# Kernel tuning notes

Measured on AMD Instinct MI355X. Metric: run time of the kernel, lower is better.

Reference implementation:

```python
import jax, jax.numpy as jnp
import numpy as np
import math

IN_C, OUT_C, K, STYLE_DIM = 512, 512, 3, 512
BATCH, H, W = 16, 64, 64
EPS = 1e-8
CONV_SCALE = 1.0 / math.sqrt(IN_C * K * K)   # fan_in scale
MOD_SCALE = 1.0 / math.sqrt(STYLE_DIM)       # EqualLinear scale (lr_mul=1)


def setup_inputs() -> dict:
    key = jax.random.key(0)
    k1, k2, k3, k4 = jax.random.split(key, 4)
    return {
        "input": jax.random.normal(k1, (BATCH, IN_C, H, W), dtype=jnp.float32),
        "style": jax.random.normal(k2, (BATCH, STYLE_DIM), dtype=jnp.float32),
        "weight": jax.random.normal(k3, (1, OUT_C, IN_C, K, K), dtype=jnp.float32),
        "mod_weight": jax.random.normal(k4, (IN_C, STYLE_DIM), dtype=jnp.float32),
        "mod_bias": jnp.ones((IN_C,), dtype=jnp.float32),  # bias_init=1
    }


def reference(input, style, weight, mod_weight, mod_bias):
    b = input.shape[0]
    # EqualLinear modulation: style -> per-sample per-in-channel scale
    s = style @ (mod_weight * MOD_SCALE).T + mod_bias          # [B, IN_C]
    # Modulate base weight per sample
    w = CONV_SCALE * weight * s[:, None, :, None, None]        # [B, OUT_C, IN_C, K, K]
    # Demodulation
    demod = jax.lax.rsqrt(jnp.sum(w * w, axis=(2, 3, 4)) + EPS)  # [B, OUT_C]
    w = w * demod[:, :, None, None, None]
    # Grouped conv with groups=batch == per-sample conv; vmap over batch
    pad = K // 2

    def conv_one(x, wk):
        # x: [IN_C, H, W], wk: [OUT_C, IN_C, K, K]
        y = jax.lax.conv_general_dilated(
            x[None], wk, window_strides=(1, 1),
            padding=[(pad, pad), (pad, pad)],
            dimension_numbers=("NCHW", "OIHW", "NCHW"))
        return y[0]

    out = jax.vmap(conv_one)(input, w)                          # [B, OUT_C, H, W]
    return out
```

## Files before the change

kernel.cpp:

```cpp
#include <hip/hip_runtime.h>

#define IN_C 512
#define OUT_C 512
#define BATCH 16
#define NPX 4096

using bf16x8 = __attribute__((ext_vector_type(8))) __bf16;
using f32x4  = __attribute__((ext_vector_type(4))) float;

static constexpr float kConvScale = 0.014731391274719739f;
static constexpr float kModScale  = 0.04419417382415922f;
static constexpr float kEps       = 1e-8f;

#define WT_TILE_BYTES (9 * 64 * 64)

__global__ void style_k(const float* __restrict__ style, const float* __restrict__ mw,
                        const float* __restrict__ mb, float* __restrict__ s) {
  __shared__ float st[IN_C];
  const int b = blockIdx.x, t = threadIdx.x;
  st[t] = style[b * IN_C + t];
  __syncthreads();
  const float4* row = (const float4*)(mw + (size_t)t * IN_C);
  float acc = 0.f;
  #pragma unroll 4
  for (int i = 0; i < IN_C / 4; i++) {
    float4 v = row[i];
    float4 u = *(const float4*)(st + i * 4);
    acc += v.x * u.x + v.y * u.y + v.z * u.z + v.w * u.w;
  }
  s[b * IN_C + t] = acc * kModScale + mb[t];
}

__global__ void wprep_k(const float* __restrict__ w, float* __restrict__ wsq,
                        char* __restrict__ wsw) {
  const int idx = blockIdx.x * 256 + threadIdx.x;
  const int ic = idx & (IN_C - 1), oc = idx >> 9;
  const int ot = oc >> 6, ocl = oc & 63, ics = ic >> 5, icl = ic & 31;
  char* tile = wsw + (size_t)(ics * 8 + ot) * WT_TILE_BYTES;
  const float* p = w + (size_t)(oc * IN_C + ic) * 9;
  float q = 0.f;
  #pragma unroll
  for (int t = 0; t < 9; t++) {
    float v = p[t];
    q += v * v;
    int B = ((t * 64 + ocl) << 6) + icl * 2;
    int Bsw = B ^ (((B >> 7) & 7) << 4);
    *(__bf16*)(tile + Bsw) = (__bf16)v;
  }
  wsq[oc * IN_C + ic] = q;
}

__global__ void demod_k(const float* __restrict__ s, const float* __restrict__ wsq,
                        float* __restrict__ dsc) {
  __shared__ float s2[IN_C];
  const int b = blockIdx.x, t = threadIdx.x;
  float sv = s[b * IN_C + t];
  s2[t] = sv * sv;
  __syncthreads();
  const float4* row = (const float4*)(wsq + (size_t)t * IN_C);
  float acc = 0.f;
  #pragma unroll 4
  for (int i = 0; i < IN_C / 4; i++) {
    float4 v = row[i];
    float4 u = *(const float4*)(s2 + i * 4);
    acc += v.x * u.x + v.y * u.y + v.z * u.z + v.w * u.w;
  }
  dsc[b * OUT_C + t] = kConvScale * rsqrtf(kConvScale * kConvScale * acc + kEps);
}

__global__ void modx_k(const float* __restrict__ x, const float* __restrict__ s,
                       __bf16* __restrict__ xm) {
  __shared__ __bf16 tile[64][73];
  const int t = threadIdx.x;
  const int bid = blockIdx.x;
  const int ict = bid & 7, pt = (bid >> 3) & 63, b = bid >> 9;
  const int ic0 = ict * 64, p0 = pt * 64;
  #pragma unroll
  for (int it = 0; it < 16; it++) {
    int idx = it * 256 + t;
    int pl = idx & 63, icl = idx >> 6;
    int ic = ic0 + icl;
    float v = x[((size_t)b * IN_C + ic) * NPX + p0 + pl] * s[b * IN_C + ic];
    tile[icl][pl] = (__bf16)v;
  }
  __syncthreads();
  #pragma unroll
  for (int it = 0; it < 2; it++) {
    int idx = it * 256 + t;
    int icb = idx & 7, pl = idx >> 3;
    alignas(16) __bf16 tmp[8];
    #pragma unroll
    for (int j = 0; j < 8; j++) tmp[j] = tile[icb * 8 + j][pl];
    *(uint4*)(xm + ((size_t)b * NPX + p0 + pl) * IN_C + ic0 + icb * 8) = *(const uint4*)tmp;
  }
}


#define XROW 4224

#define SGB __builtin_amdgcn_sched_group_barrier
#define SGB_MIX() { SGB(0x100, 3, 0); SGB(0x8, 8, 0); SGB(0x100, 3, 0); SGB(0x8, 8, 0); \
                    SGB(0x100, 3, 0); SGB(0x8, 8, 0); SGB(0x100, 3, 0); SGB(0x8, 8, 0); }
#define SGB_MFMA() { SGB(0x8, 8, 0); SGB(0x8, 8, 0); SGB(0x8, 8, 0); SGB(0x8, 8, 0); }

__global__ __launch_bounds__(256, 2)
void conv_k(const __bf16* __restrict__ xm, const char* __restrict__ wsw,
            const float* __restrict__ dsc, float* __restrict__ out) {
  __shared__ __align__(16) char xsb[10 * XROW];
  __shared__ __align__(16) char wsb[WT_TILE_BYTES];

  const int tid = threadIdx.x;
  const int lane = tid & 63;
  const int wn = tid >> 6;
  const int l15 = lane & 15, kb8 = lane >> 4;
  const int bid = blockIdx.x;
  const int pt = bid & 7, ot = (bid >> 3) & 7, b = bid >> 6;
  const int h0 = pt * 8, oc0 = ot * 64;

  if (tid < 80) {
    int r = tid >> 3, side = (tid >> 2) & 1, ch = tid & 3;
    uint4 z = {0, 0, 0, 0};
    *(uint4*)(xsb + r * XROW + side * 65 * 64 + ch * 16) = z;
  }
  if (h0 == 0) {
    uint4 z = {0, 0, 0, 0};
    for (int i = tid; i < 264; i += 256) ((uint4*)xsb)[i] = z;
  }
  if (h0 == 56) {
    uint4 z = {0, 0, 0, 0};
    for (int i = tid; i < 264; i += 256) ((uint4*)(xsb + 9 * XROW))[i] = z;
  }

  #define XGLDS(ICS)                                                          \
    {                                                                         \
      _Pragma("unroll")                                                       \
      for (int r = 0; r < 10; r++) {                                          \
        int h = h0 + r - 1;                                                   \
        if ((unsigned)h < 64u)                                                \
          __builtin_amdgcn_global_load_lds(                                   \
              (const __attribute__((address_space(1))) void*)(xm +            \
                  ((size_t)(b * 4096 + h * 64 + (tid >> 2))) * 512 +          \
                  (ICS) * 32 + (tid & 3) * 8),                                \
              (__attribute__((address_space(3))) void*)(xsb +                 \
                  r * XROW + 64 + tid * 16),                                  \
              16, 0, 0);                                                      \
      }                                                                       \
    }
  #define WGLDS(ICS)                                                          \
    {                                                                         \
      const char* wt = wsw + (size_t)((ICS) * 8 + ot) * WT_TILE_BYTES;        \
      _Pragma("unroll")                                                       \
      for (int g = 0; g < 9; g++) {                                           \
        int off = (g * 256 + tid) * 16;                                       \
        __builtin_amdgcn_global_load_lds(                                     \
            (const __attribute__((address_space(1))) void*)(wt + off),        \
            (__attribute__((address_space(3))) void*)(wsb + off), 16, 0, 0);  \
      }                                                                       \
    }

  f32x4 acc[4][8];
  #pragma unroll
  for (int i = 0; i < 4; i++)
    #pragma unroll
    for (int j = 0; j < 8; j++) acc[i][j] = f32x4{0.f, 0.f, 0.f, 0.f};

  const int swz = ((l15 >> 1) & 7) << 4;
  const int wrd_base = ((l15 << 6) + kb8 * 16) ^ swz;

  bf16x8 afA[4], bfA[8], afB[4], bfB[8];
  #define LOADT(T, AF, BF)                                                    \
    {                                                                         \
      _Pragma("unroll")                                                       \
      for (int fm = 0; fm < 4; fm++)                                          \
        AF[fm] = *(const bf16x8*)(wsb + ((T) * 4096 + fm * 1024 + wrd_base)); \
      _Pragma("unroll")                                                       \
      for (int fn = 0; fn < 8; fn++) {                                        \
        int px = wn * 128 + fn * 16 + l15;                                    \
        BF[fn] = *(const bf16x8*)(xsb + ((px >> 6) + ((T) / 3)) * XROW +      \
                                  ((px & 63) + ((T) % 3)) * 64 + kb8 * 16);   \
      }                                                                       \
    }
  #define MFMAT(AF, BF)                                                       \
    {                                                                         \
      _Pragma("unroll")                                                       \
      for (int fm = 0; fm < 4; fm++)                                          \
        _Pragma("unroll")                                                     \
        for (int fn = 0; fn < 8; fn++)                                        \
          acc[fm][fn] = __builtin_amdgcn_mfma_f32_16x16x32_bf16(              \
              AF[fm], BF[fn], acc[fm][fn], 0, 0, 0);                          \
    }

  for (int s = 0; s < 16; s++) {
    __syncthreads();
    XGLDS(s)
    WGLDS(s)
    __syncthreads();

    LOADT(0, afA, bfA)
    LOADT(1, afB, bfB)
    MFMAT(afA, bfA)  SGB_MIX()
    LOADT(2, afA, bfA)
    MFMAT(afB, bfB)  SGB_MIX()
    LOADT(3, afB, bfB)
    MFMAT(afA, bfA)  SGB_MIX()
    LOADT(4, afA, bfA)
    MFMAT(afB, bfB)  SGB_MIX()
    LOADT(5, afB, bfB)
    MFMAT(afA, bfA)  SGB_MIX()
    LOADT(6, afA, bfA)
    MFMAT(afB, bfB)  SGB_MIX()
    LOADT(7, afB, bfB)
    MFMAT(afA, bfA)  SGB_MIX()
    LOADT(8, afA, bfA)
    MFMAT(afB, bfB)  SGB_MIX()
    MFMAT(afA, bfA)  SGB_MFMA()
  }

  #pragma unroll
  for (int fm = 0; fm < 4; fm++) {
    #pragma unroll
    for (int j = 0; j < 4; j++) {
      int oc = oc0 + fm * 16 + kb8 * 4 + j;
      float dm = dsc[b * OUT_C + oc];
      float* orow = out + ((size_t)b * OUT_C + oc) * NPX + h0 * 64;
      #pragma unroll
      for (int fn = 0; fn < 8; fn++) {
        int px = wn * 128 + fn * 16 + l15;
        orow[px] = acc[fm][fn][j] * dm;
      }
    }
  }
}

extern "C" void kernel_launch(void* const* d_in, const int* in_sizes, int n_in,
                              void* d_out, int out_size, void* d_ws, size_t ws_size,
                              hipStream_t stream) {
  const float* input  = (const float*)d_in[0];
  const float* style  = (const float*)d_in[1];
  const float* weight = (const float*)d_in[2];
  const float* mod_w  = (const float*)d_in[3];
  const float* mod_b  = (const float*)d_in[4];
  float* out = (float*)d_out;

  char* p = (char*)d_ws;
  float* s    = (float*)p;  p += (size_t)BATCH * IN_C * 4;
  float* dsc  = (float*)p;  p += (size_t)BATCH * OUT_C * 4;
  float* wsq  = (float*)p;  p += (size_t)OUT_C * IN_C * 4;
  char*  wsw  = p;          p += (size_t)16 * 8 * WT_TILE_BYTES;
  __bf16* xm  = (__bf16*)p;

  style_k<<<BATCH, 512, 0, stream>>>(style, mod_w, mod_b, s);
  wprep_k<<<1024, 256, 0, stream>>>(weight, wsq, wsw);
  demod_k<<<BATCH, 512, 0, stream>>>(s, wsq, dsc);
  modx_k<<<BATCH * 8 * 64, 256, 0, stream>>>(input, s, xm);
  conv_k<<<BATCH * 8 * 8, 256, 0, stream>>>(xm, wsw, dsc, out);
}
```

Measured before the change: 348.1 us.

## Double-buffer LDS tiles to overlap global loads with MFMA compute

Input and weight LDS tiles are now double-buffered: each iteration issues the async global-to-LDS loads for the next channel slice while computing on the current one, with one barrier per iteration instead of two. The goal is to hide global memory latency behind the MFMA work. It doubles LDS use, so launch bounds drop to one block per SM-equivalent, lowering occupancy. Nothing explicitly waits for the async loads to complete before the barrier, so correctness relies on how the barrier handles outstanding loads.

```diff
diff --git a/kernel.cpp b/kernel.cpp
--- a/kernel.cpp
+++ b/kernel.cpp
@@ -97,17 +97,18 @@
 
 
 #define XROW 4224
+#define XBUF (10 * XROW)
 
 #define SGB __builtin_amdgcn_sched_group_barrier
 #define SGB_MIX() { SGB(0x100, 3, 0); SGB(0x8, 8, 0); SGB(0x100, 3, 0); SGB(0x8, 8, 0); \
                     SGB(0x100, 3, 0); SGB(0x8, 8, 0); SGB(0x100, 3, 0); SGB(0x8, 8, 0); }
 #define SGB_MFMA() { SGB(0x8, 8, 0); SGB(0x8, 8, 0); SGB(0x8, 8, 0); SGB(0x8, 8, 0); }
 
-__global__ __launch_bounds__(256, 2)
+__global__ __launch_bounds__(256, 1)
 void conv_k(const __bf16* __restrict__ xm, const char* __restrict__ wsw,
             const float* __restrict__ dsc, float* __restrict__ out) {
-  __shared__ __align__(16) char xsb[10 * XROW];
-  __shared__ __align__(16) char wsb[WT_TILE_BYTES];
+  __shared__ __align__(16) char xsb[2 * XBUF];
+  __shared__ __align__(16) char wsb[2 * WT_TILE_BYTES];
 
   const int tid = threadIdx.x;
   const int lane = tid & 63;
@@ -117,21 +118,23 @@
   const int pt = bid & 7, ot = (bid >> 3) & 7, b = bid >> 6;
   const int h0 = pt * 8, oc0 = ot * 64;
 
-  if (tid < 80) {
-    int r = tid >> 3, side = (tid >> 2) & 1, ch = tid & 3;
+  if (tid < 160) {
+    int bb = tid / 80, rr = (tid % 80) >> 3, side = (tid >> 2) & 1, ch = tid & 3;
     uint4 z = {0, 0, 0, 0};
-    *(uint4*)(xsb + r * XROW + side * 65 * 64 + ch * 16) = z;
+    *(uint4*)(xsb + bb * XBUF + rr * XROW + side * 65 * 64 + ch * 16) = z;
   }
   if (h0 == 0) {
     uint4 z = {0, 0, 0, 0};
-    for (int i = tid; i < 264; i += 256) ((uint4*)xsb)[i] = z;
+    for (int i = tid; i < 2 * 264; i += 256)
+      *((uint4*)(xsb + (i >= 264 ? XBUF : 0)) + (i % 264)) = z;
   }
   if (h0 == 56) {
     uint4 z = {0, 0, 0, 0};
-    for (int i = tid; i < 264; i += 256) ((uint4*)(xsb + 9 * XROW))[i] = z;
-  }
-
-  #define XGLDS(ICS)                                                          \
+    for (int i = tid; i < 2 * 264; i += 256)
+      *((uint4*)(xsb + (i >= 264 ? XBUF : 0) + 9 * XROW) + (i % 264)) = z;
+  }
+
+  #define XGLDS(ICS, XB)                                                      \
     {                                                                         \
       _Pragma("unroll")                                                       \
       for (int r = 0; r < 10; r++) {                                          \
@@ -141,12 +144,12 @@
               (const __attribute__((address_space(1))) void*)(xm +            \
                   ((size_t)(b * 4096 + h * 64 + (tid >> 2))) * 512 +          \
                   (ICS) * 32 + (tid & 3) * 8),                                \
-              (__attribute__((address_space(3))) void*)(xsb +                 \
+              (__attribute__((address_space(3))) void*)((XB) +                \
                   r * XROW + 64 + tid * 16),                                  \
               16, 0, 0);                                                      \
       }                                                                       \
     }
-  #define WGLDS(ICS)                                                          \
+  #define WGLDS(ICS, WB)                                                      \
     {                                                                         \
       const char* wt = wsw + (size_t)((ICS) * 8 + ot) * WT_TILE_BYTES;        \
       _Pragma("unroll")                                                       \
@@ -154,7 +157,7 @@
         int off = (g * 256 + tid) * 16;                                       \
         __builtin_amdgcn_global_load_lds(                                     \
             (const __attribute__((address_space(1))) void*)(wt + off),        \
-            (__attribute__((address_space(3))) void*)(wsb + off), 16, 0, 0);  \
+            (__attribute__((address_space(3))) void*)((WB) + off), 16, 0, 0); \
       }                                                                       \
     }
 
@@ -172,11 +175,11 @@
     {                                                                         \
       _Pragma("unroll")                                                       \
       for (int fm = 0; fm < 4; fm++)                                          \
-        AF[fm] = *(const bf16x8*)(wsb + ((T) * 4096 + fm * 1024 + wrd_base)); \
+        AF[fm] = *(const bf16x8*)(wcur + ((T) * 4096 + fm * 1024 + wrd_base));\
       _Pragma("unroll")                                                       \
       for (int fn = 0; fn < 8; fn++) {                                        \
         int px = wn * 128 + fn * 16 + l15;                                    \
-        BF[fn] = *(const bf16x8*)(xsb + ((px >> 6) + ((T) / 3)) * XROW +      \
+        BF[fn] = *(const bf16x8*)(xcur + ((px >> 6) + ((T) / 3)) * XROW +     \
                                   ((px & 63) + ((T) % 3)) * 64 + kb8 * 16);   \
       }                                                                       \
     }
@@ -190,11 +193,20 @@
               AF[fm], BF[fn], acc[fm][fn], 0, 0, 0);                          \
     }
 
+  XGLDS(0, xsb)
+  WGLDS(0, wsb)
+  __syncthreads();
+
   for (int s = 0; s < 16; s++) {
-    __syncthreads();
-    XGLDS(s)
-    WGLDS(s)
-    __syncthreads();
+    const char* xcur = xsb + (s & 1) * XBUF;
+    const char* wcur = wsb + (s & 1) * WT_TILE_BYTES;
+    char* xnxt = xsb + ((s + 1) & 1) * XBUF;
+    char* wnxt = wsb + ((s + 1) & 1) * WT_TILE_BYTES;
+
+    if (s < 15) {
+      XGLDS(s + 1, xnxt)
+      WGLDS(s + 1, wnxt)
+    }
 
     LOADT(0, afA, bfA)
     LOADT(1, afB, bfB)
@@ -214,6 +226,8 @@
     LOADT(8, afA, bfA)
     MFMAT(afB, bfB)  SGB_MIX()
     MFMAT(afA, bfA)  SGB_MFMA()
+
+    __syncthreads();
   }
 
   #pragma unroll
```

Result: slower. 374.2 us (+7.5%).

## Switch conv inner loop to 32x32x16 bf16 MFMA with swizzled LDS layout

Applied to the files above, without the earlier changes.

Replaces the 16x16x32 MFMA tiling with 32x32x16 MFMAs (2 OC tiles x 4 pixel tiles per wave, split into two K chunks). LDS fragment reads for both weights and the activation halo tile are reworked with an XOR swizzle, and the global-to-LDS activation load permutes channel chunks to match. The goal is fewer MFMA issues and fewer LDS reads per FLOP, along with fewer bank conflicts. The cost is a more complex addressing scheme that must exactly match the weight pre-swizzle, plus changed scheduling-barrier groupings.

```diff
diff --git a/kernel.cpp b/kernel.cpp
--- a/kernel.cpp
+++ b/kernel.cpp
@@ -7,6 +7,7 @@
 
 using bf16x8 = __attribute__((ext_vector_type(8))) __bf16;
 using f32x4  = __attribute__((ext_vector_type(4))) float;
+using f32x16 = __attribute__((ext_vector_type(16))) float;
 
 static constexpr float kConvScale = 0.014731391274719739f;
 static constexpr float kModScale  = 0.04419417382415922f;
@@ -97,11 +98,10 @@
 
 
 #define XROW 4224
-
 #define SGB __builtin_amdgcn_sched_group_barrier
-#define SGB_MIX() { SGB(0x100, 3, 0); SGB(0x8, 8, 0); SGB(0x100, 3, 0); SGB(0x8, 8, 0); \
-                    SGB(0x100, 3, 0); SGB(0x8, 8, 0); SGB(0x100, 3, 0); SGB(0x8, 8, 0); }
-#define SGB_MFMA() { SGB(0x8, 8, 0); SGB(0x8, 8, 0); SGB(0x8, 8, 0); SGB(0x8, 8, 0); }
+#define SGB_MIX() { SGB(0x100, 3, 0); SGB(0x8, 4, 0); SGB(0x100, 3, 0); SGB(0x8, 4, 0); \
+                    SGB(0x100, 3, 0); SGB(0x8, 4, 0); SGB(0x100, 3, 0); SGB(0x8, 4, 0); }
+#define SGB_MFMA() { SGB(0x8, 4, 0); SGB(0x8, 4, 0); SGB(0x8, 4, 0); SGB(0x8, 4, 0); }
 
 __global__ __launch_bounds__(256, 2)
 void conv_k(const __bf16* __restrict__ xm, const char* __restrict__ wsw,
@@ -112,7 +112,7 @@
   const int tid = threadIdx.x;
   const int lane = tid & 63;
   const int wn = tid >> 6;
-  const int l15 = lane & 15, kb8 = lane >> 4;
+  const int l31 = lane & 31, hi = lane >> 5;
   const int bid = blockIdx.x;
   const int pt = bid & 7, ot = (bid >> 3) & 7, b = bid >> 6;
   const int h0 = pt * 8, oc0 = ot * 64;
@@ -131,6 +131,7 @@
     for (int i = tid; i < 264; i += 256) ((uint4*)(xsb + 9 * XROW))[i] = z;
   }
 
+  const int chv = ((tid & 3) ^ ((((tid >> 2) + 1) >> 1) & 3)) * 8;
   #define XGLDS(ICS)                                                          \
     {                                                                         \
       _Pragma("unroll")                                                       \
@@ -140,7 +141,7 @@
           __builtin_amdgcn_global_load_lds(                                   \
               (const __attribute__((address_space(1))) void*)(xm +            \
                   ((size_t)(b * 4096 + h * 64 + (tid >> 2))) * 512 +          \
-                  (ICS) * 32 + (tid & 3) * 8),                                \
+                  (ICS) * 32 + chv),                                          \
               (__attribute__((address_space(3))) void*)(xsb +                 \
                   r * XROW + 64 + tid * 16),                                  \
               16, 0, 0);                                                      \
@@ -158,36 +159,54 @@
       }                                                                       \
     }
 
-  f32x4 acc[4][8];
-  #pragma unroll
-  for (int i = 0; i < 4; i++)
-    #pragma unroll
-    for (int j = 0; j < 8; j++) acc[i][j] = f32x4{0.f, 0.f, 0.f, 0.f};
-
-  const int swz = ((l15 >> 1) & 7) << 4;
-  const int wrd_base = ((l15 << 6) + kb8 * 16) ^ swz;
+  f32x16 acc[2][4];
+  #pragma unroll
+  for (int o = 0; o < 2; o++)
+    #pragma unroll
+    for (int p = 0; p < 4; p++)
+      #pragma unroll
+      for (int i = 0; i < 16; i++) acc[o][p][i] = 0.f;
+
+  const int swzA = ((l31 >> 1) & 7) << 4;
+  const int wrdA = ((l31 << 6) + (hi << 4)) ^ swzA;
+
+  int xb[12];
+  #pragma unroll
+  for (int p = 0; p < 4; p++)
+    #pragma unroll
+    for (int d = 0; d < 3; d++) {
+      int slot = (p & 1) * 32 + l31 + d;
+      int f = (slot >> 1) & 3;
+      xb[p * 3 + d] = (wn * 2 + (p >> 1)) * XROW + slot * 64 +
+                      ((hi ^ (f & 1)) << 4) + ((f >> 1) << 5);
+    }
 
   bf16x8 afA[4], bfA[8], afB[4], bfB[8];
   #define LOADT(T, AF, BF)                                                    \
     {                                                                         \
       _Pragma("unroll")                                                       \
-      for (int fm = 0; fm < 4; fm++)                                          \
-        AF[fm] = *(const bf16x8*)(wsb + ((T) * 4096 + fm * 1024 + wrd_base)); \
-      _Pragma("unroll")                                                       \
-      for (int fn = 0; fn < 8; fn++) {                                        \
-        int px = wn * 128 + fn * 16 + l15;                                    \
-        BF[fn] = *(const bf16x8*)(xsb + ((px >> 6) + ((T) / 3)) * XROW +      \
-                                  ((px & 63) + ((T) % 3)) * 64 + kb8 * 16);   \
-      }                                                                       \
+      for (int oct = 0; oct < 2; oct++)                                       \
+        _Pragma("unroll")                                                     \
+        for (int kc = 0; kc < 2; kc++)                                        \
+          AF[oct * 2 + kc] = *(const bf16x8*)(wsb + (T) * 4096 +              \
+              oct * 2048 + (wrdA ^ (kc << 5)));                               \
+      _Pragma("unroll")                                                       \
+      for (int pxt = 0; pxt < 4; pxt++)                                       \
+        _Pragma("unroll")                                                     \
+        for (int kc = 0; kc < 2; kc++)                                        \
+          BF[pxt * 2 + kc] = *(const bf16x8*)(xsb + ((T) / 3) * XROW +        \
+              (xb[pxt * 3 + (T) % 3] ^ (kc << 5)));                           \
     }
   #define MFMAT(AF, BF)                                                       \
     {                                                                         \
       _Pragma("unroll")                                                       \
-      for (int fm = 0; fm < 4; fm++)                                          \
+      for (int kc = 0; kc < 2; kc++)                                          \
         _Pragma("unroll")                                                     \
-        for (int fn = 0; fn < 8; fn++)                                        \
-          acc[fm][fn] = __builtin_amdgcn_mfma_f32_16x16x32_bf16(              \
-              AF[fm], BF[fn], acc[fm][fn], 0, 0, 0);                          \
+        for (int oct = 0; oct < 2; oct++)                                     \
+          _Pragma("unroll")                                                   \
+          for (int pxt = 0; pxt < 4; pxt++)                                   \
+            acc[oct][pxt] = __builtin_amdgcn_mfma_f32_32x32x16_bf16(          \
+                AF[oct * 2 + kc], BF[pxt * 2 + kc], acc[oct][pxt], 0, 0, 0);  \
     }
 
   for (int s = 0; s < 16; s++) {
@@ -217,16 +236,16 @@
   }
 
   #pragma unroll
-  for (int fm = 0; fm < 4; fm++) {
-    #pragma unroll
-    for (int j = 0; j < 4; j++) {
-      int oc = oc0 + fm * 16 + kb8 * 4 + j;
+  for (int oct = 0; oct < 2; oct++) {
+    #pragma unroll
+    for (int reg = 0; reg < 16; reg++) {
+      int oc = oc0 + oct * 32 + (reg & 3) + 8 * (reg >> 2) + hi * 4;
       float dm = dsc[b * OUT_C + oc];
       float* orow = out + ((size_t)b * OUT_C + oc) * NPX + h0 * 64;
       #pragma unroll
-      for (int fn = 0; fn < 8; fn++) {
-        int px = wn * 128 + fn * 16 + l15;
-        orow[px] = acc[fm][fn][j] * dm;
+      for (int pxt = 0; pxt < 4; pxt++) {
+        int px = wn * 128 + pxt * 32 + l31;
+        orow[px] = acc[oct][pxt][reg] * dm;
       }
     }
   }
```

New measurement: 358.2 us. 1.03x slower.
